# Kernel tuning notes

Measured on AMD Instinct MI355X. Metric: run time of the kernel, lower is better.

## Reference

```python
import jax, jax.numpy as jnp
import numpy as np

D_MODEL = 1024
N_HEADS = 16
D_FF = 4096
EPS = 1e-6


def layernorm(x, alpha, bias):
    # torch.std uses Bessel correction (ddof=1)
    mean = jnp.mean(x, axis=-1, keepdims=True)
    std = jnp.std(x, axis=-1, keepdims=True, ddof=1)
    return alpha * (x - mean) / (std + EPS) + bias


def setup_inputs() -> dict:
    key = jax.random.key(0)
    ks = jax.random.split(key, 12)
    s = 1.0 / np.sqrt(D_MODEL)
    sf = 1.0 / np.sqrt(D_FF)
    return {
        "x": jax.random.normal(ks[0], (2, 2048, D_MODEL), jnp.float32),
        "mask": jnp.ones((2, 1, 1, 2048), jnp.int32),
        "wq": jax.random.normal(ks[1], (D_MODEL, D_MODEL), jnp.float32) * s,
        "wk": jax.random.normal(ks[2], (D_MODEL, D_MODEL), jnp.float32) * s,
        "wv": jax.random.normal(ks[3], (D_MODEL, D_MODEL), jnp.float32) * s,
        "wo": jax.random.normal(ks[4], (D_MODEL, D_MODEL), jnp.float32) * s,
        "wo_b": jnp.zeros((D_MODEL,), jnp.float32),
        "w1": jax.random.normal(ks[5], (D_MODEL, D_FF), jnp.float32) * s,
        "b1": jnp.zeros((D_FF,), jnp.float32),
        "w2": jax.random.normal(ks[6], (D_FF, D_MODEL), jnp.float32) * sf,
        "b2": jnp.zeros((D_MODEL,), jnp.float32),
        "alpha1": jnp.ones((D_MODEL,), jnp.float32),
        "bias1": jnp.zeros((D_MODEL,), jnp.float32),
        "alpha2": jnp.ones((D_MODEL,), jnp.float32),
        "bias2": jnp.zeros((D_MODEL,), jnp.float32),
    }


def reference(x, mask, wq, wk, wv, wo, wo_b, w1, b1, w2, b2,
              alpha1, bias1, alpha2, bias2):
    B, S, D = x.shape
    h, dk = N_HEADS, D_MODEL // N_HEADS
    # projections -> [B, h, S, dk]
    q = (x @ wq).reshape(B, S, h, dk).transpose(0, 2, 1, 3)
    k = (x @ wk).reshape(B, S, h, dk).transpose(0, 2, 1, 3)
    v = (x @ wv).reshape(B, S, h, dk).transpose(0, 2, 1, 3)
    scores = jnp.einsum('bhqd,bhkd->bhqk', q, k) / jnp.sqrt(jnp.float32(dk))
    scores = jnp.where(mask == 0, jnp.float32(-1e9), scores)
    attn = jax.nn.softmax(scores, axis=-1)
    ctx = jnp.einsum('bhqk,bhkd->bhqd', attn, v)
    ctx = ctx.transpose(0, 2, 1, 3).reshape(B, S, D)
    attn_out = ctx @ wo + wo_b
    x = layernorm(x + attn_out, alpha1, bias1)
    ff = jax.nn.relu(x @ w1 + b1) @ w2 + b2
    x = layernorm(x + ff, alpha2, bias2)
    return x
```

## Files before the change

### kernel.cpp

```cpp
#include <hip/hip_runtime.h>
#include <hip/hip_bf16.h>

#define D_MODEL 1024
#define N_HEADS 16
#define DK      64
#define SEQ     2048
#define BATCH   2
#define D_FF    4096
#define ROWS    (BATCH*SEQ)
#define LN_EPS  1e-6f
#define KTILE   128

typedef __hip_bfloat16 bf16;
typedef __attribute__((ext_vector_type(8))) short frag8;
typedef __attribute__((ext_vector_type(4))) float facc4;

__device__ inline float bf2f(unsigned short u){ return __uint_as_float(((unsigned)u) << 16); }
__device__ inline float toF(bf16 v){ return __bfloat162float(v); }
__device__ inline unsigned short f2bu(float f){ bf16 h = __float2bfloat16(f); return *reinterpret_cast<unsigned short*>(&h); }

__device__ inline unsigned cvtpk_bf16(float lo, float hi){
    unsigned r;
    asm("v_cvt_pk_bf16_f32 %0, %1, %2" : "=v"(r) : "v"(lo), "v"(hi));
    return r;
}

__device__ inline float ld1(const void* p, size_t idx, bool f32) {
    return f32 ? ((const float*)p)[idx] : toF(((const bf16*)p)[idx]);
}

struct U8 { unsigned short v[8]; };
__device__ inline U8 ld8bf(const void* p, size_t idx, bool f32) {
    U8 r;
    if (!f32) {
        *reinterpret_cast<uint4*>(r.v) = *reinterpret_cast<const uint4*>((const unsigned short*)p + idx);
    } else {
        const float* f = (const float*)p + idx;
        const float4 a = *reinterpret_cast<const float4*>(f);
        const float4 b = *reinterpret_cast<const float4*>(f + 4);
        r.v[0]=f2bu(a.x); r.v[1]=f2bu(a.y); r.v[2]=f2bu(a.z); r.v[3]=f2bu(a.w);
        r.v[4]=f2bu(b.x); r.v[5]=f2bu(b.y); r.v[6]=f2bu(b.z); r.v[7]=f2bu(b.w);
    }
    return r;
}

__device__ inline void ld8f(const void* p, int idx, bool f32, float* o) {
    if (!f32) {
        uint4 u = *reinterpret_cast<const uint4*>((const unsigned short*)p + idx);
        const unsigned short* us = reinterpret_cast<const unsigned short*>(&u);
        #pragma unroll
        for (int j = 0; j < 8; ++j) o[j] = bf2f(us[j]);
    } else {
        const float* f = (const float*)p + idx;
        const float4 a = *reinterpret_cast<const float4*>(f);
        const float4 b = *reinterpret_cast<const float4*>(f + 4);
        o[0]=a.x; o[1]=a.y; o[2]=a.z; o[3]=a.w;
        o[4]=b.x; o[5]=b.y; o[6]=b.z; o[7]=b.w;
    }
}

__device__ inline void gld16(const void* g, void* l) {
    __builtin_amdgcn_global_load_lds(
        reinterpret_cast<const __attribute__((address_space(1))) void*>(
            reinterpret_cast<uintptr_t>(g)),
        reinterpret_cast<__attribute__((address_space(3))) void*>(
            (unsigned int)reinterpret_cast<uintptr_t>(l)),
        16, 0, 0);
}

__global__ void probe_kernel(const void* __restrict__ xp, int* __restrict__ flag) {
    __shared__ int hit;
    if (threadIdx.x == 0) hit = 0;
    __syncthreads();
    const bf16* p = (const bf16*)xp;
    int bad = 0;
    for (int i = threadIdx.x; i < 8192; i += 256) {
        float v = fabsf(toF(p[i]));
        if (!(v <= 1e5f)) bad = 1;
    }
    if (bad) atomicOr(&hit, 1);
    __syncthreads();
    if (threadIdx.x == 0) *flag = hit;
}

__global__ __launch_bounds__(256) void xcvt_kernel(const void* __restrict__ x,
    bf16* __restrict__ out, const int* __restrict__ flagp)
{
    const bool f32 = (*flagp) != 0;
    const size_t i = ((size_t)blockIdx.x * 256 + threadIdx.x) * 8;
    U8 d = ld8bf(x, i, f32);
    *reinterpret_cast<uint4*>(out + i) = *reinterpret_cast<const uint4*>(d.v);
}

__device__ inline void ttile(const void* W, bf16* WT, int K, int N,
                             int n0, int k0, bool f32, float (*tile)[65], int t)
{
    const int lr = t >> 2;
    const int lc = (t & 3) * 16;
    if (!f32) {
        const unsigned short* src = (const unsigned short*)W + (size_t)(k0 + lr) * N + n0 + lc;
        uint4 u0 = *reinterpret_cast<const uint4*>(src);
        uint4 u1 = *reinterpret_cast<const uint4*>(src + 8);
        const unsigned short* us0 = reinterpret_cast<const unsigned short*>(&u0);
        const unsigned short* us1 = reinterpret_cast<const unsigned short*>(&u1);
        #pragma unroll
        for (int j = 0; j < 8; ++j) {
            tile[lr][lc + j]     = bf2f(us0[j]);
            tile[lr][lc + 8 + j] = bf2f(us1[j]);
        }
    } else {
        const float* src = (const float*)W + (size_t)(k0 + lr) * N + n0 + lc;
        #pragma unroll
        for (int q4 = 0; q4 < 4; ++q4) {
            const float4 f = *reinterpret_cast<const float4*>(src + 4 * q4);
            tile[lr][lc + 4*q4 + 0] = f.x;
            tile[lr][lc + 4*q4 + 1] = f.y;
            tile[lr][lc + 4*q4 + 2] = f.z;
            tile[lr][lc + 4*q4 + 3] = f.w;
        }
    }
    __syncthreads();
    unsigned short o[16];
    #pragma unroll
    for (int j = 0; j < 16; ++j) o[j] = f2bu(tile[lc + j][lr]);
    bf16* dst = WT + (size_t)(n0 + lr) * K + k0 + lc;
    *reinterpret_cast<uint4*>(dst)     = *reinterpret_cast<const uint4*>(&o[0]);
    *reinterpret_cast<uint4*>(dst + 8) = *reinterpret_cast<const uint4*>(&o[8]);
}

__global__ __launch_bounds__(256) void transpose_kernel(const void* __restrict__ W,
    bf16* __restrict__ WT, int K, int N, const int* __restrict__ flagp)
{
    __shared__ float tile[64][65];
    ttile(W, WT, K, N, blockIdx.x * 64, blockIdx.y * 64, (*flagp) != 0, tile, threadIdx.x);
}

__global__ __launch_bounds__(256) void transpose4_kernel(const void* __restrict__ w0,
    const void* __restrict__ w1, const void* __restrict__ w2, const void* __restrict__ w3,
    bf16* __restrict__ WT4, const int* __restrict__ flagp)
{
    const int which = blockIdx.z;
    const void* W = (which == 0) ? w0 : (which == 1) ? w1 : (which == 2) ? w2 : w3;
    bf16* WT = WT4 + (size_t)which * D_MODEL * D_MODEL;
    __shared__ float tile[64][65];
    ttile(W, WT, D_MODEL, D_MODEL, blockIdx.x * 64, blockIdx.y * 64, (*flagp) != 0, tile, threadIdx.x);
}

__global__ __launch_bounds__(256) void transposeFF_kernel(const void* __restrict__ w1,
    const void* __restrict__ w2, bf16* __restrict__ W1T, bf16* __restrict__ W2T,
    const int* __restrict__ flagp)
{
    __shared__ float tile[64][65];
    const int z = blockIdx.y, bid = blockIdx.x;
    const void* W = z ? w2 : w1;
    bf16* WT = z ? W2T : W1T;
    const int K = z ? D_FF : D_MODEL;
    const int N = z ? D_MODEL : D_FF;
    const int n0 = (z ? (bid & 15) : (bid & 63)) * 64;
    const int k0 = (z ? (bid >> 4) : (bid >> 6)) * 64;
    ttile(W, WT, K, N, n0, k0, (*flagp) != 0, tile, threadIdx.x);
}

template<bool RELU, bool BIAS, int NMAT, int SPLITK>
__global__ __launch_bounds__(256) void mgemm_kernel(const bf16* __restrict__ A,
    const bf16* __restrict__ BT, const void* __restrict__ bias,
    bf16* __restrict__ C, int M, int N, int K, const int* __restrict__ flagp)
{
    const bool inF32 = (*flagp) != 0;

    __shared__ unsigned short sA[128 * 64];
    __shared__ unsigned short sB[128 * 64];

    int which = 0, colb = blockIdx.x;
    if (NMAT > 1) { which = blockIdx.x >> 3; colb = blockIdx.x & 7; }
    const int kslice = (SPLITK > 1) ? blockIdx.z : 0;
    const int Kspan  = K / SPLITK;
    const int kbase  = kslice * Kspan;
    const bf16* Bp = BT + (size_t)which * N * K;
    bf16*       Cp = C  + (size_t)which * M * N + (size_t)kslice * M * N;

    const int row0 = blockIdx.y * 128;
    const int col0 = colb * 128;

    const int t    = threadIdx.x;
    const int wave = t >> 6;
    const int lane = t & 63;
    const int lm   = lane & 15;
    const int q    = lane >> 4;
    const int wm   = (wave & 1) * 64;
    const int wn   = (wave >> 1) * 64;

    facc4 acc[4][4];
    #pragma unroll
    for (int i = 0; i < 4; ++i)
        #pragma unroll
        for (int j = 0; j < 4; ++j)
            acc[i][j] = (facc4){0.f, 0.f, 0.f, 0.f};

    for (int k0 = kbase; k0 < kbase + Kspan; k0 += 64) {
        __syncthreads();
        #pragma unroll
        for (int j = 0; j < 4; ++j) {
            const int ch = (wave * 4 + j) * 64 + lane;
            const int r  = ch >> 3;
            const int cs = ch & 7;
            const int c  = cs ^ (r & 7);
            gld16(A  + (size_t)(row0 + r) * K + k0 + 8 * c, &sA[(wave * 4 + j) * 512]);
            gld16(Bp + (size_t)(col0 + r) * K + k0 + 8 * c, &sB[(wave * 4 + j) * 512]);
        }
        __syncthreads();

        #pragma unroll
        for (int kk = 0; kk < 64; kk += 32) {
            const int cr = (kk >> 3) + q;
            frag8 af[4], bfr[4];
            #pragma unroll
            for (int im = 0; im < 4; ++im) {
                const int m = wm + 16 * im + lm;
                af[im] = *reinterpret_cast<const frag8*>(&sA[m * 64 + ((cr ^ (m & 7)) << 3)]);
            }
            #pragma unroll
            for (int in = 0; in < 4; ++in) {
                const int n = wn + 16 * in + lm;
                bfr[in] = *reinterpret_cast<const frag8*>(&sB[n * 64 + ((cr ^ (n & 7)) << 3)]);
            }
            #pragma unroll
            for (int im = 0; im < 4; ++im)
                #pragma unroll
                for (int in = 0; in < 4; ++in)
                    acc[im][in] = __builtin_amdgcn_mfma_f32_16x16x32_bf16(af[im], bfr[in], acc[im][in], 0, 0, 0);
        }
    }

    if (NMAT > 1 && which == 2) {
        #pragma unroll
        for (int in = 0; in < 4; ++in) {
            const int col = col0 + wn + 16*in + lm;
            const int hh = col >> 6, dd = col & 63;
            #pragma unroll
            for (int im = 0; im < 4; ++im) {
                const int rowb = row0 + wm + 16*im + 4*q;
                const int bb = rowb >> 11, ss = rowb & 2047;
                union { uint2 v; unsigned u[2]; } ov;
                ov.u[0] = cvtpk_bf16(acc[im][in][0], acc[im][in][1]);
                ov.u[1] = cvtpk_bf16(acc[im][in][2], acc[im][in][3]);
                *reinterpret_cast<uint2*>(Cp + ((size_t)((bb * 16 + hh) * 64 + dd)) * 2048 + ss) = ov.v;
            }
        }
        return;
    }

    #pragma unroll
    for (int in = 0; in < 4; ++in) {
        const int col = col0 + wn + 16*in + lm;
        float bv = 0.f;
        if (BIAS && kslice == 0) bv = ld1(bias, col, inF32);
        #pragma unroll
        for (int im = 0; im < 4; ++im) {
            #pragma unroll
            for (int r = 0; r < 4; ++r) {
                const int row = row0 + wm + 16*im + 4*q + r;
                float v = acc[im][in][r] + bv;
                if (RELU) v = fmaxf(v, 0.f);
                Cp[(size_t)row * N + col] = __float2bfloat16(v);
            }
        }
    }
}

__global__ __launch_bounds__(256, 2) void fattn_kernel(
    const bf16* __restrict__ Qg, const bf16* __restrict__ Kg,
    const bf16* __restrict__ VTg, const int* __restrict__ mask,
    bf16* __restrict__ ctx)
{
    __shared__ unsigned short sK[2][128 * 64];
    __shared__ unsigned short sV[2][64 * 128];
    __shared__ __align__(16) float madd[SEQ];

    const int t    = threadIdx.x;
    const int lin  = blockIdx.x + 16 * (blockIdx.y + 16 * blockIdx.z);
    const int rid  = (lin & 7) * 64 + (lin >> 3);
    const int qt   = rid & 15;
    const int h    = (rid >> 4) & 15;
    const int b    = rid >> 8;
    const int q0   = qt * 128;
    const int bh   = b * N_HEADS + h;
    const int wave = t >> 6;
    const int lane = t & 63;
    const int lm   = lane & 15;
    const int qd   = lane >> 4;
    const bool qo  = (qd & 1) != 0;

    const float SCL = 0.18033688011112042f;

    auto stage = [&](int bi, int kt) {
        const int k0 = kt * KTILE;
        #pragma unroll
        for (int j = 0; j < 4; ++j) {
            const int ch = (wave * 4 + j) * 64 + lane;
            const int rK = ch >> 3, cK = (ch & 7) ^ (rK & 7);
            gld16(Kg + ((size_t)(b * SEQ + k0 + rK)) * D_MODEL + h * DK + 8 * cK,
                  &sK[bi][(wave * 4 + j) * 512]);
            const int rV = ch >> 4, cV = (ch & 15) ^ (rV & 15);
            gld16(VTg + ((size_t)(bh * DK + rV)) * SEQ + k0 + 8 * cV,
                  &sV[bi][(wave * 4 + j) * 512]);
        }
    };

    stage(0, 0);
    #pragma unroll
    for (int i = 0; i < SEQ / (256 * 4); ++i) {
        const int idx = (i * 256 + t) * 4;
        const int4 mv = *reinterpret_cast<const int4*>(&mask[b * SEQ + idx]);
        madd[idx + 0] = (mv.x == 0) ? -1.442695e9f : 0.f;
        madd[idx + 1] = (mv.y == 0) ? -1.442695e9f : 0.f;
        madd[idx + 2] = (mv.z == 0) ? -1.442695e9f : 0.f;
        madd[idx + 3] = (mv.w == 0) ? -1.442695e9f : 0.f;
    }

    frag8 qf[2][2];
    #pragma unroll
    for (int s = 0; s < 2; ++s) {
        const bf16* qsrc = Qg + ((size_t)(b * SEQ + q0 + 32 * wave + 16 * s + lm)) * D_MODEL + h * DK;
        qf[s][0] = *reinterpret_cast<const frag8*>(qsrc + 8 * qd);
        qf[s][1] = *reinterpret_cast<const frag8*>(qsrc + 32 + 8 * qd);
    }

    facc4 accO[2][4];
    #pragma unroll
    for (int s = 0; s < 2; ++s)
        #pragma unroll
        for (int in = 0; in < 4; ++in) accO[s][in] = (facc4){0.f, 0.f, 0.f, 0.f};
    float m_r[2] = {-1e30f, -1e30f}, l_r[2] = {0.f, 0.f};

    for (int kt = 0; kt < SEQ / KTILE; ++kt) {
        const int cur = kt & 1;
        const int k0  = kt * KTILE;
        __syncthreads();
        if (kt + 1 < SEQ / KTILE) stage(cur ^ 1, kt + 1);

        facc4 accST[2][8];
        #pragma unroll
        for (int s = 0; s < 2; ++s)
            #pragma unroll
            for (int i = 0; i < 8; ++i) accST[s][i] = (facc4){0.f, 0.f, 0.f, 0.f};
        __builtin_amdgcn_s_setprio(1);
        #pragma unroll
        for (int i = 0; i < 8; ++i) {
            #pragma unroll
            for (int s2 = 0; s2 < 2; ++s2) {
                const int cr = 4 * s2 + qd;
                frag8 kf = *reinterpret_cast<const frag8*>(
                    &sK[cur][(16 * i + lm) * 64 + ((cr ^ (lm & 7)) << 3)]);
                accST[0][i] = __builtin_amdgcn_mfma_f32_16x16x32_bf16(kf, qf[0][s2], accST[0][i], 0, 0, 0);
                accST[1][i] = __builtin_amdgcn_mfma_f32_16x16x32_bf16(kf, qf[1][s2], accST[1][i], 0, 0, 0);
            }
        }
        __builtin_amdgcn_s_setprio(0);

        facc4 vmx[2];
        #pragma unroll
        for (int s = 0; s < 2; ++s) vmx[s] = (facc4){-1e30f, -1e30f, -1e30f, -1e30f};
        #pragma unroll
        for (int i = 0; i < 8; ++i) {
            const facc4 mv = *reinterpret_cast<const facc4*>(&madd[k0 + 16 * i + 4 * qd]);
            #pragma unroll
            for (int s = 0; s < 2; ++s) {
                #pragma unroll
                for (int r = 0; r < 4; ++r) {
                    accST[s][i][r] = fmaf(accST[s][i][r], SCL, mv[r]);
                    vmx[s][r] = fmaxf(vmx[s][r], accST[s][i][r]);
                }
            }
        }
        float mn[2], alpha[2] = {1.f, 1.f};
        bool resc[2];
        #pragma unroll
        for (int s = 0; s < 2; ++s) {
            const float mloc = fmaxf(fmaxf(vmx[s][0], vmx[s][1]), fmaxf(vmx[s][2], vmx[s][3]));
            const bool skip = __all(mloc - m_r[s] <= 11.54f) != 0;
            resc[s] = !skip;
            if (skip) {
                mn[s] = m_r[s];
            } else {
                float m0 = mloc;
                m0 = fmaxf(m0, __shfl_xor(m0, 16));
                m0 = fmaxf(m0, __shfl_xor(m0, 32));
                mn[s] = fmaxf(m_r[s], m0);
                alpha[s] = __builtin_amdgcn_exp2f(m_r[s] - mn[s]);
                m_r[s] = mn[s];
            }
        }

        unsigned up[2][8][2];
        facc4 ps4[2];
        #pragma unroll
        for (int s = 0; s < 2; ++s) ps4[s] = (facc4){0.f, 0.f, 0.f, 0.f};
        #pragma unroll
        for (int s = 0; s < 2; ++s) {
            #pragma unroll
            for (int i = 0; i < 8; ++i) {
                const float p0 = __builtin_amdgcn_exp2f(accST[s][i][0] - mn[s]);
                const float p1 = __builtin_amdgcn_exp2f(accST[s][i][1] - mn[s]);
                const float p2 = __builtin_amdgcn_exp2f(accST[s][i][2] - mn[s]);
                const float p3 = __builtin_amdgcn_exp2f(accST[s][i][3] - mn[s]);
                ps4[s][0] += p0; ps4[s][1] += p1; ps4[s][2] += p2; ps4[s][3] += p3;
                up[s][i][0] = cvtpk_bf16(p0, p1);
                up[s][i][1] = cvtpk_bf16(p2, p3);
            }
        }
        #pragma unroll
        for (int s = 0; s < 2; ++s) {
            float ps = (ps4[s][0] + ps4[s][1]) + (ps4[s][2] + ps4[s][3]);
            ps += __shfl_xor(ps, 16);
            ps += __shfl_xor(ps, 32);
            if (resc[s]) {
                l_r[s] = l_r[s] * alpha[s] + ps;
                #pragma unroll
                for (int in = 0; in < 4; ++in)
                    #pragma unroll
                    for (int r = 0; r < 4; ++r) accO[s][in][r] *= alpha[s];
            } else {
                l_r[s] += ps;
            }
        }

        __builtin_amdgcn_s_setprio(1);
        #pragma unroll
        for (int c = 0; c < 4; ++c) {
            union { frag8 f; unsigned u[4]; } pf0_, pf1_;
            #pragma unroll
            for (int s = 0; s < 2; ++s) {
                unsigned a0 = up[s][2*c][0],     a1 = up[s][2*c][1];
                unsigned b0 = up[s][2*c + 1][0], b1 = up[s][2*c + 1][1];
                asm("v_permlane32_swap_b32 %0, %1" : "+v"(a0), "+v"(b0));
                asm("v_permlane32_swap_b32 %0, %1" : "+v"(a1), "+v"(b1));
                const unsigned t0 = qo ? a0 : b0;
                const unsigned t1 = qo ? a1 : b1;
                const unsigned r0 = __shfl_xor(t0, 16);
                const unsigned r1 = __shfl_xor(t1, 16);
                unsigned u0 = qo ? r0 : a0;
                unsigned u1 = qo ? r1 : a1;
                unsigned u2 = qo ? b0 : r0;
                unsigned u3 = qo ? b1 : r1;
                if (s == 0) { pf0_.u[0]=u0; pf0_.u[1]=u1; pf0_.u[2]=u2; pf0_.u[3]=u3; }
                else        { pf1_.u[0]=u0; pf1_.u[1]=u1; pf1_.u[2]=u2; pf1_.u[3]=u3; }
            }
            #pragma unroll
            for (int in = 0; in < 4; ++in) {
                const int cr = 4 * c + qd;
                frag8 vf = *reinterpret_cast<const frag8*>(
                    &sV[cur][(16 * in + lm) * 128 + ((cr ^ lm) << 3)]);
                accO[0][in] = __builtin_amdgcn_mfma_f32_16x16x32_bf16(vf, pf0_.f, accO[0][in], 0, 0, 0);
                accO[1][in] = __builtin_amdgcn_mfma_f32_16x16x32_bf16(vf, pf1_.f, accO[1][in], 0, 0, 0);
            }
        }
        __builtin_amdgcn_s_setprio(0);
    }

    #pragma unroll
    for (int s = 0; s < 2; ++s) {
        const float invl = 1.f / l_r[s];
        bf16* crow = ctx + ((size_t)(b * SEQ + q0 + 32 * wave + 16 * s + lm)) * D_MODEL + h * DK;
        #pragma unroll
        for (int in = 0; in < 4; ++in) {
            union { uint2 v; unsigned u[2]; } ov;
            ov.u[0] = cvtpk_bf16(accO[s][in][0] * invl, accO[s][in][1] * invl);
            ov.u[1] = cvtpk_bf16(accO[s][in][2] * invl, accO[s][in][3] * invl);
            *reinterpret_cast<uint2*>(crow + 16 * in + 4 * qd) = ov.v;
        }
    }
}

template<bool BASE_WS, bool OUT_WS>
__global__ __launch_bounds__(128) void ln_kernel(const void* __restrict__ base,
    const bf16* __restrict__ addv, const bf16* __restrict__ addv2,
    const void* __restrict__ alpha, const void* __restrict__ bias,
    void* __restrict__ outp, const int* __restrict__ flagp)
{
    const bool inF32 = (*flagp) != 0;
    __shared__ float red[2];
    __shared__ float red2[2];
    const int row = blockIdx.x, t = threadIdx.x;
    const size_t off = (size_t)row * D_MODEL + t * 8;

    float v[8];
    {
        const U8 bz = ld8bf(base, off, BASE_WS ? false : inF32);
        uint4 a1 = *reinterpret_cast<const uint4*>(addv + off);
        const unsigned short* a1s = reinterpret_cast<const unsigned short*>(&a1);
        #pragma unroll
        for (int j = 0; j < 8; ++j) v[j] = bf2f(bz.v[j]) + bf2f(a1s[j]);
        if (addv2) {
            uint4 a2 = *reinterpret_cast<const uint4*>(addv2 + off);
            const unsigned short* a2s = reinterpret_cast<const unsigned short*>(&a2);
            #pragma unroll
            for (int j = 0; j < 8; ++j) v[j] += bf2f(a2s[j]);
        }
    }

    float s = ((v[0]+v[1]) + (v[2]+v[3])) + ((v[4]+v[5]) + (v[6]+v[7]));
    #pragma unroll
    for (int o = 1; o < 64; o <<= 1) s += __shfl_xor(s, o);
    if ((t & 63) == 0) red[t >> 6] = s;
    __syncthreads();
    const float mean = (red[0] + red[1]) * (1.f / (float)D_MODEL);

    float sq = 0.f;
    #pragma unroll
    for (int j = 0; j < 8; ++j) { const float d = v[j] - mean; sq += d * d; }
    #pragma unroll
    for (int o = 1; o < 64; o <<= 1) sq += __shfl_xor(sq, o);
    if ((t & 63) == 0) red2[t >> 6] = sq;
    __syncthreads();
    const float var = (red2[0] + red2[1]) * (1.f / (float)(D_MODEL - 1));
    const float inv = 1.f / (sqrtf(var) + LN_EPS);

    float av[8], bv[8];
    ld8f(alpha, t * 8, inF32, av);
    ld8f(bias,  t * 8, inF32, bv);
    float y[8];
    #pragma unroll
    for (int j = 0; j < 8; ++j)
        y[j] = av[j] * (v[j] - mean) * inv + bv[j];

    if (OUT_WS || !inF32) {
        union { uint4 u; unsigned w[4]; } o_;
        o_.w[0] = cvtpk_bf16(y[0], y[1]);
        o_.w[1] = cvtpk_bf16(y[2], y[3]);
        o_.w[2] = cvtpk_bf16(y[4], y[5]);
        o_.w[3] = cvtpk_bf16(y[6], y[7]);
        *reinterpret_cast<uint4*>((bf16*)outp + off) = o_.u;
    } else {
        float* op = (float*)outp + off;
        const float4 f0 = {y[0], y[1], y[2], y[3]};
        const float4 f1 = {y[4], y[5], y[6], y[7]};
        *reinterpret_cast<float4*>(op)     = f0;
        *reinterpret_cast<float4*>(op + 4) = f1;
    }
}

extern "C" void kernel_launch(void* const* d_in, const int* in_sizes, int n_in,
                              void* d_out, int out_size, void* d_ws, size_t ws_size,
                              hipStream_t stream)
{
    const void* x    = d_in[0];
    const int*  mask = (const int*)d_in[1];
    const void* wq   = d_in[2];
    const void* wk   = d_in[3];
    const void* wv   = d_in[4];
    const void* wo   = d_in[5];
    const void* wo_b = d_in[6];
    const void* w1   = d_in[7];
    const void* b1   = d_in[8];
    const void* w2   = d_in[9];
    const void* b2   = d_in[10];
    const void* al1  = d_in[11];
    const void* bi1  = d_in[12];
    const void* al2  = d_in[13];
    const void* bi2  = d_in[14];

    const size_t MB = 1024 * 1024;
    char* ws = (char*)d_ws;
    const bool BIG = ws_size >= 64 * MB + 4096;
    if (!BIG && ws_size < 56 * MB + 4096) return;

    if (BIG) {
        bf16* Qb   = (bf16*)(ws + 0 * MB);
        bf16* VTb  = (bf16*)(ws + 16 * MB);
        bf16* Xb   = (bf16*)(ws + 24 * MB);
        bf16* Kb   = (bf16*)(ws + 8 * MB);
        bf16* WT4  = (bf16*)(ws + 32 * MB);
        bf16* WOT  = WT4 + (size_t)3 * D_MODEL * D_MODEL;
        bf16* W1T  = (bf16*)(ws + 40 * MB);
        bf16* W2T  = (bf16*)(ws + 48 * MB);
        bf16* CTXb = (bf16*)(ws + 56 * MB);
        bf16* ATT0 = (bf16*)(ws + 0 * MB);
        bf16* ATT1 = (bf16*)(ws + 8 * MB);
        bf16* X1b  = (bf16*)(ws + 56 * MB);
        bf16* FFb  = (bf16*)(ws + 0 * MB);
        bf16* X20  = (bf16*)(ws + 32 * MB);
        bf16* X21  = (bf16*)(ws + 40 * MB);
        int*  flagp = (int*)(ws + 64 * MB);

        probe_kernel<<<1, 256, 0, stream>>>(x, flagp);
        xcvt_kernel<<<dim3(ROWS * D_MODEL / 2048), 256, 0, stream>>>(x, Xb, flagp);

        transpose4_kernel<<<dim3(16, 16, 4), 256, 0, stream>>>(wq, wk, wv, wo, WT4, flagp);
        transposeFF_kernel<<<dim3(1024, 2), 256, 0, stream>>>(w1, w2, W1T, W2T, flagp);

        mgemm_kernel<false, false, 3, 1><<<dim3(24, 32), 256, 0, stream>>>(
            Xb, WT4, nullptr, Qb, ROWS, D_MODEL, D_MODEL, flagp);

        fattn_kernel<<<dim3(SEQ / 128, N_HEADS, BATCH), 256, 0, stream>>>(Qb, Kb, VTb, mask, CTXb);

        mgemm_kernel<false, true, 1, 2><<<dim3(8, 32, 2), 256, 0, stream>>>(
            CTXb, WOT, wo_b, ATT0, ROWS, D_MODEL, D_MODEL, flagp);
        ln_kernel<false, true><<<ROWS, 128, 0, stream>>>(x, ATT0, ATT1, al1, bi1, X1b, flagp);

        mgemm_kernel<true, true, 1, 1><<<dim3(32, 32), 256, 0, stream>>>(
            X1b, W1T, b1, FFb, ROWS, D_FF, D_MODEL, flagp);

        mgemm_kernel<false, true, 1, 2><<<dim3(8, 32, 2), 256, 0, stream>>>(
            FFb, W2T, b2, X20, ROWS, D_MODEL, D_FF, flagp);
        ln_kernel<true, false><<<ROWS, 128, 0, stream>>>(X1b, X20, X21, al2, bi2, d_out, flagp);
    } else {
        bf16* Qb    = (bf16*)(ws + 0 * MB);
        bf16* Kb    = (bf16*)(ws + 8 * MB);
        bf16* VTb   = (bf16*)(ws + 16 * MB);
        bf16* Xb    = (bf16*)(ws + 24 * MB);
        bf16* WQKVT = (bf16*)(ws + 32 * MB);
        bf16* CTXb  = (bf16*)(ws + 32 * MB);
        bf16* W2T   = (bf16*)(ws + 32 * MB);
        bf16* WOT   = (bf16*)(ws + 0 * MB);
        bf16* ATT0  = (bf16*)(ws + 48 * MB);
        bf16* W1T   = (bf16*)(ws + 48 * MB);
        bf16* X20   = (bf16*)(ws + 48 * MB);
        bf16* X1b   = (bf16*)(ws + 40 * MB);
        bf16* FFb   = (bf16*)(ws + 0 * MB);
        int*  flagp = (int*)(ws + 56 * MB);

        probe_kernel<<<1, 256, 0, stream>>>(x, flagp);
        xcvt_kernel<<<dim3(ROWS * D_MODEL / 2048), 256, 0, stream>>>(x, Xb, flagp);

        transpose_kernel<<<dim3(16, 16), 256, 0, stream>>>(wq, WQKVT,           D_MODEL, D_MODEL, flagp);
        transpose_kernel<<<dim3(16, 16), 256, 0, stream>>>(wk, WQKVT + 1048576, D_MODEL, D_MODEL, flagp);
        transpose_kernel<<<dim3(16, 16), 256, 0, stream>>>(wv, WQKVT + 2097152, D_MODEL, D_MODEL, flagp);

        mgemm_kernel<false, false, 3, 1><<<dim3(24, 32), 256, 0, stream>>>(
            Xb, WQKVT, nullptr, Qb, ROWS, D_MODEL, D_MODEL, flagp);

        fattn_kernel<<<dim3(SEQ / 128, N_HEADS, BATCH), 256, 0, stream>>>(Qb, Kb, VTb, mask, CTXb);

        transpose_kernel<<<dim3(16, 16), 256, 0, stream>>>(wo, WOT, D_MODEL, D_MODEL, flagp);
        mgemm_kernel<false, true, 1, 1><<<dim3(8, 32), 256, 0, stream>>>(
            CTXb, WOT, wo_b, ATT0, ROWS, D_MODEL, D_MODEL, flagp);
        ln_kernel<false, true><<<ROWS, 128, 0, stream>>>(x, ATT0, nullptr, al1, bi1, X1b, flagp);

        transpose_kernel<<<dim3(64, 16), 256, 0, stream>>>(w1, W1T, D_MODEL, D_FF, flagp);
        mgemm_kernel<true, true, 1, 1><<<dim3(32, 32), 256, 0, stream>>>(
            X1b, W1T, b1, FFb, ROWS, D_FF, D_MODEL, flagp);

        transpose_kernel<<<dim3(16, 64), 256, 0, stream>>>(w2, W2T, D_FF, D_MODEL, flagp);
        mgemm_kernel<false, true, 1, 1><<<dim3(8, 32), 256, 0, stream>>>(
            FFb, W2T, b2, X20, ROWS, D_MODEL, D_FF, flagp);
        ln_kernel<true, false><<<ROWS, 128, 0, stream>>>(X1b, X20, nullptr, al2, bi2, d_out, flagp);
    }
}
```

Measured before the change: 360.9 us.

## Merge prep kernels into one launch and remap GEMM blocks for XCD locality

New measurement: 363.5 us. No clear change (+0.7%).

```diff
diff --git a/kernel.cpp b/kernel.cpp
--- a/kernel.cpp
+++ b/kernel.cpp
@@ -135,30 +135,41 @@
     ttile(W, WT, K, N, blockIdx.x * 64, blockIdx.y * 64, (*flagp) != 0, tile, threadIdx.x);
 }
 
-__global__ __launch_bounds__(256) void transpose4_kernel(const void* __restrict__ w0,
-    const void* __restrict__ w1, const void* __restrict__ w2, const void* __restrict__ w3,
-    bf16* __restrict__ WT4, const int* __restrict__ flagp)
-{
-    const int which = blockIdx.z;
-    const void* W = (which == 0) ? w0 : (which == 1) ? w1 : (which == 2) ? w2 : w3;
-    bf16* WT = WT4 + (size_t)which * D_MODEL * D_MODEL;
+__global__ __launch_bounds__(256) void prep_kernel(
+    const void* __restrict__ x, bf16* __restrict__ Xb,
+    const void* __restrict__ wq, const void* __restrict__ wk,
+    const void* __restrict__ wv, const void* __restrict__ wo, bf16* __restrict__ WT4,
+    const void* __restrict__ w1, const void* __restrict__ w2,
+    bf16* __restrict__ W1T, bf16* __restrict__ W2T,
+    const int* __restrict__ flagp)
+{
     __shared__ float tile[64][65];
-    ttile(W, WT, D_MODEL, D_MODEL, blockIdx.x * 64, blockIdx.y * 64, (*flagp) != 0, tile, threadIdx.x);
-}
-
-__global__ __launch_bounds__(256) void transposeFF_kernel(const void* __restrict__ w1,
-    const void* __restrict__ w2, bf16* __restrict__ W1T, bf16* __restrict__ W2T,
-    const int* __restrict__ flagp)
-{
-    __shared__ float tile[64][65];
-    const int z = blockIdx.y, bid = blockIdx.x;
+    const bool f32 = (*flagp) != 0;
+    const int id = blockIdx.x;
+    if (id < 2048) {
+        const size_t i = ((size_t)id * 256 + threadIdx.x) * 8;
+        U8 d = ld8bf(x, i, f32);
+        *reinterpret_cast<uint4*>(Xb + i) = *reinterpret_cast<const uint4*>(d.v);
+        return;
+    }
+    if (id < 3072) {
+        const int local = id - 2048;
+        const int which = local >> 8;
+        const void* W = (which == 0) ? wq : (which == 1) ? wk : (which == 2) ? wv : wo;
+        bf16* WT = WT4 + (size_t)which * D_MODEL * D_MODEL;
+        const int rem = local & 255;
+        ttile(W, WT, D_MODEL, D_MODEL, (rem & 15) * 64, (rem >> 4) * 64, f32, tile, threadIdx.x);
+        return;
+    }
+    const int local = id - 3072;
+    const int z = local >> 10, bid = local & 1023;
     const void* W = z ? w2 : w1;
     bf16* WT = z ? W2T : W1T;
     const int K = z ? D_FF : D_MODEL;
     const int N = z ? D_MODEL : D_FF;
     const int n0 = (z ? (bid & 15) : (bid & 63)) * 64;
     const int k0 = (z ? (bid >> 4) : (bid >> 6)) * 64;
-    ttile(W, WT, K, N, n0, k0, (*flagp) != 0, tile, threadIdx.x);
+    ttile(W, WT, K, N, n0, k0, f32, tile, threadIdx.x);
 }
 
 template<bool RELU, bool BIAS, int NMAT, int SPLITK>
@@ -171,15 +182,24 @@
     __shared__ unsigned short sA[128 * 64];
     __shared__ unsigned short sB[128 * 64];
 
-    int which = 0, colb = blockIdx.x;
-    if (NMAT > 1) { which = blockIdx.x >> 3; colb = blockIdx.x & 7; }
-    const int kslice = (SPLITK > 1) ? blockIdx.z : 0;
+    const int gx  = gridDim.x, gy = gridDim.y;
+    const int nwg = gx * gy * gridDim.z;
+    const int lin = blockIdx.x + gx * (blockIdx.y + gy * blockIdx.z);
+    const int rid = (lin & 7) * (nwg >> 3) + (lin >> 3);
+    const int by  = rid % gy;
+    const int tq  = rid / gy;
+    const int bx  = tq % gx;
+    const int bz  = tq / gx;
+
+    int which = 0, colb = bx;
+    if (NMAT > 1) { which = bx >> 3; colb = bx & 7; }
+    const int kslice = (SPLITK > 1) ? bz : 0;
     const int Kspan  = K / SPLITK;
     const int kbase  = kslice * Kspan;
     const bf16* Bp = BT + (size_t)which * N * K;
     bf16*       Cp = C  + (size_t)which * M * N + (size_t)kslice * M * N;
 
-    const int row0 = blockIdx.y * 128;
+    const int row0 = by * 128;
     const int col0 = colb * 128;
 
     const int t    = threadIdx.x;
@@ -567,9 +587,9 @@
 
     if (BIG) {
         bf16* Qb   = (bf16*)(ws + 0 * MB);
+        bf16* Kb   = (bf16*)(ws + 8 * MB);
         bf16* VTb  = (bf16*)(ws + 16 * MB);
         bf16* Xb   = (bf16*)(ws + 24 * MB);
-        bf16* Kb   = (bf16*)(ws + 8 * MB);
         bf16* WT4  = (bf16*)(ws + 32 * MB);
         bf16* WOT  = WT4 + (size_t)3 * D_MODEL * D_MODEL;
         bf16* W1T  = (bf16*)(ws + 40 * MB);
@@ -584,10 +604,8 @@
         int*  flagp = (int*)(ws + 64 * MB);
 
         probe_kernel<<<1, 256, 0, stream>>>(x, flagp);
-        xcvt_kernel<<<dim3(ROWS * D_MODEL / 2048), 256, 0, stream>>>(x, Xb, flagp);
-
-        transpose4_kernel<<<dim3(16, 16, 4), 256, 0, stream>>>(wq, wk, wv, wo, WT4, flagp);
-        transposeFF_kernel<<<dim3(1024, 2), 256, 0, stream>>>(w1, w2, W1T, W2T, flagp);
+        prep_kernel<<<dim3(5120), 256, 0, stream>>>(x, Xb, wq, wk, wv, wo, WT4,
+                                                    w1, w2, W1T, W2T, flagp);
 
         mgemm_kernel<false, false, 3, 1><<<dim3(24, 32), 256, 0, stream>>>(
             Xb, WT4, nullptr, Qb, ROWS, D_MODEL, D_MODEL, flagp);
```
